# Kernel optimization log

Measured on AMD Instinct MI355X. Metric: run time of the kernel, lower is better.

## Reference

```python
import jax, jax.numpy as jnp
import numpy as np

STRIDE = 16
PRE_K = 600
POST_K = 100
NMS_T = 0.7


def _gen_anchors(base=16.0, ratios=(0.5, 1.0, 2.0), scales=(8.0, 16.0, 32.0)):
    a = []
    for s in scales:
        for r in ratios:
            w = base * s * (r ** 0.5)
            h = base * s / (r ** 0.5)
            a.append([-w / 2, -h / 2, w / 2, h / 2])
    return jnp.asarray(a, jnp.float32)  # [9,4]


def _conv(x, w, b, pad):
    y = jax.lax.conv_general_dilated(x, w, (1, 1), [(pad, pad), (pad, pad)],
                                     dimension_numbers=("NCHW", "OIHW", "NCHW"))
    return y + b[None, :, None, None]


def _decode(deltas, anchors):
    w = anchors[:, 2] - anchors[:, 0]
    h = anchors[:, 3] - anchors[:, 1]
    cx = anchors[:, 0] + 0.5 * w
    cy = anchors[:, 1] + 0.5 * h
    dx, dy, dw, dh = deltas[:, 0], deltas[:, 1], deltas[:, 2], deltas[:, 3]
    pcx = cx + dx * w
    pcy = cy + dy * h
    pw = w * jnp.exp(dw)
    ph = h * jnp.exp(dh)
    return jnp.stack([pcx - 0.5 * pw, pcy - 0.5 * ph,
                      pcx + 0.5 * pw, pcy + 0.5 * ph], axis=-1)


def _nms_keep(boxes, thresh):
    # boxes already sorted by score descending; returns bool keep mask [N]
    x1, y1, x2, y2 = boxes[:, 0], boxes[:, 1], boxes[:, 2], boxes[:, 3]
    area = (x2 - x1) * (y2 - y1)
    xx1 = jnp.maximum(x1[:, None], x1[None, :])
    yy1 = jnp.maximum(y1[:, None], y1[None, :])
    xx2 = jnp.minimum(x2[:, None], x2[None, :])
    yy2 = jnp.minimum(y2[:, None], y2[None, :])
    inter = jnp.maximum(xx2 - xx1, 0.0) * jnp.maximum(yy2 - yy1, 0.0)
    iou = inter / (area[:, None] + area[None, :] - inter)
    n = boxes.shape[0]
    idx = jnp.arange(n)

    def body(i, keep):
        suppress = keep[i] & (iou[i] > thresh) & (idx > i)
        return keep & ~suppress

    return jax.lax.fori_loop(0, n, body, jnp.ones((n,), bool))


def setup_inputs() -> dict:
    key = jax.random.key(0)
    ks = jax.random.split(key, 7)
    C_in, C_mid, A = 256, 256, 9
    feats = jax.random.normal(ks[0], (4, C_in, 128, 128), jnp.float32)
    conv_w = jax.random.normal(ks[1], (C_mid, C_in, 3, 3), jnp.float32) * 0.02
    conv_b = jnp.zeros((C_mid,), jnp.float32)
    cls_w = jax.random.normal(ks[2], (A, C_mid, 1, 1), jnp.float32) * 0.05
    cls_b = jnp.zeros((A,), jnp.float32)
    bbox_w = jax.random.normal(ks[3], (A * 4, C_mid, 1, 1), jnp.float32) * 0.02
    bbox_b = jnp.zeros((A * 4,), jnp.float32)
    return {"features": feats, "conv_w": conv_w, "conv_b": conv_b,
            "cls_w": cls_w, "cls_b": cls_b, "bbox_w": bbox_w, "bbox_b": bbox_b,
            "image_h": 2048, "image_w": 2048}


def reference(features, conv_w, conv_b, cls_w, cls_b, bbox_w, bbox_b, image_h, image_w):
    B, _, H, W = features.shape
    A = cls_w.shape[0]
    t = jax.nn.relu(_conv(features, conv_w, conv_b, 1))
    logits = _conv(t, cls_w, cls_b, 0)        # [B,A,H,W]
    bbox_deltas = _conv(t, bbox_w, bbox_b, 0)  # [B,4A,H,W]

    anchors = _gen_anchors()
    sx = jnp.arange(W, dtype=jnp.float32) * STRIDE
    sy = jnp.arange(H, dtype=jnp.float32) * STRIDE
    gy, gx = jnp.meshgrid(sy, sx, indexing="ij")
    shifts = jnp.stack([gx, gy, gx, gy], axis=2).reshape(-1, 4)  # [HW,4]
    anchors_all = (anchors[None, :, :] + shifts[:, None, :]).reshape(-1, 4)  # [HW*A,4]

    scores = jnp.transpose(logits, (0, 2, 3, 1)).reshape(B, -1)          # [B,HWA]
    deltas = jnp.transpose(bbox_deltas, (0, 2, 3, 1)).reshape(B, -1, 4)  # [B,HWA,4]

    img_w = jnp.float32(image_w)
    img_h = jnp.float32(image_h)

    def per_image(s, d):
        p = _decode(d, anchors_all)
        p = jnp.stack([jnp.clip(p[:, 0], 0.0, img_w),
                       jnp.clip(p[:, 1], 0.0, img_h),
                       jnp.clip(p[:, 2], 0.0, img_w),
                       jnp.clip(p[:, 3], 0.0, img_h)], axis=-1)
        _, topi = jax.lax.top_k(s, PRE_K)
        p = p[topi]                                # [PRE_K,4] sorted by score
        keep = _nms_keep(p, NMS_T)
        order = jnp.argsort(jnp.where(keep, 0, 1), stable=True)  # kept first, score order
        sel = order[:POST_K]
        valid = keep[sel]
        return p[sel] * valid[:, None].astype(p.dtype)  # zero-pad suppressed slots

    return jax.vmap(per_image)(scores, deltas)  # [B,POST_K,4]
```

## Files before the change

kernel.cpp:

```cpp
#include <hip/hip_runtime.h>
#include <cstdint>
#include <cstddef>

#define BB 4
#define CIN 256
#define HH 128
#define WW 128
#define NANCH (HH*WW*9)
#define PRE_K 600
#define POST_K 100
#define NMS_T 0.7f
#define CAND_CAP 8192
#define CCNT_STRIDE 16

typedef _Float16 f16x8 __attribute__((ext_vector_type(8)));
typedef float    f32x4 __attribute__((ext_vector_type(4)));

#define WS_SCORES 0
#define WS_DELTAS (BB*NANCH)
#define WS_WHI    (WS_DELTAS + BB*NANCH*4)
#define WS_WLO    (WS_WHI + 9*256*128)
#define WS_HIST   (WS_WLO + 9*256*128)
#define WS_CCNT   (WS_HIST + 8192)
#define WS_CAND   (WS_CCNT + 64)
#define WS_BOX6   (WS_CAND + BB*CAND_CAP*2)
#define WS_MROW   (WS_BOX6 + BB*PRE_K*4)
#define WS_PHI    (WS_MROW + BB*PRE_K*10*2)
#define WS_PLANE_F 8388608
#define WS_PLO    (WS_PHI + WS_PLANE_F)
#define WS_ZERO   (WS_PLO + WS_PLANE_F)
#define WS_TOTAL_FULL (WS_ZERO + 16)
#define WS_TOTAL_MIN  WS_PHI

__device__ inline unsigned score_key(float f) {
    unsigned u = __float_as_uint(f);
    return (u & 0x80000000u) ? ~u : (u | 0x80000000u);
}

__device__ inline void decode_box(unsigned idx, const float* __restrict__ deltas,
                                  int b, float fw, float fh, float* o4)
{
    const int a   = (int)(idx % 9u);
    const int n4  = (int)(idx / 9u);
    const int hh_ = n4 >> 7;
    const int ww_ = n4 & 127;
    const int si_ = a / 3, ri = a % 3;
    const double sq = (ri == 0) ? 0.70710678118654752440 : ((ri == 1) ? 1.0 : 1.41421356237309504880);
    const double sc = (si_ == 0) ? 8.0 : ((si_ == 1) ? 16.0 : 32.0);
    const float half_w = (float)(16.0 * sc * sq * 0.5);
    const float half_h = (float)(16.0 * sc / sq * 0.5);
    const float shx = 16.f * (float)ww_;
    const float shy = 16.f * (float)hh_;
    const float x1a = shx - half_w, x2a = shx + half_w;
    const float y1a = shy - half_h, y2a = shy + half_h;
    const float aw = x2a - x1a, ah = y2a - y1a;
    const float acx = x1a + 0.5f*aw, acy = y1a + 0.5f*ah;
    const float* d = deltas + ((size_t)b*NANCH + idx) * 4;
    const float dx = d[0], dy = d[1], dw = d[2], dh = d[3];
    const float pcx = acx + dx*aw;
    const float pcy = acy + dy*ah;
    const float pw  = aw * expf(dw);
    const float ph  = ah * expf(dh);
    o4[0] = fminf(fmaxf(pcx - 0.5f*pw, 0.f), fw);
    o4[1] = fminf(fmaxf(pcy - 0.5f*ph, 0.f), fh);
    o4[2] = fminf(fmaxf(pcx + 0.5f*pw, 0.f), fw);
    o4[3] = fminf(fmaxf(pcy + 0.5f*ph, 0.f), fh);
}

__global__ __launch_bounds__(256)
void prep_all(const float* __restrict__ feat, const float* __restrict__ convw,
              _Float16* __restrict__ pHi, _Float16* __restrict__ pLo,
              _Float16* __restrict__ whi, _Float16* __restrict__ wlo,
              float* __restrict__ zeroPg, unsigned* __restrict__ ghist,
              int prepBlocks)
{
    const int blk = blockIdx.x;
    if (blk < prepBlocks) {
        const int id = blk * 256 + threadIdx.x;
        if (blk == 0 && threadIdx.x < 16) zeroPg[threadIdx.x] = 0.f;
        const int gx = id & 127;
        const int gy = (id >> 7) & 127;
        const int ck = (id >> 14) & 7;
        const int b  = id >> 17;
        const int g  = (((gx + 1) >> 1) & 1) | (((gy + 1) & 1) << 1);
        const float* fb = feat + ((size_t)(b*256 + ck*32) << 14) + (gy << 7) + gx;
        f16x8 gh[4], gl[4];
        #pragma unroll
        for (int icg = 0; icg < 4; ++icg)
            #pragma unroll
            for (int k = 0; k < 8; ++k) {
                const float v = fb[(size_t)(icg*8 + k) << 14] * 16.f;
                const _Float16 h = (_Float16)v;
                gh[icg][k] = h;
                gl[icg][k] = (_Float16)(v - (float)h);
            }
        char* Hc = (char*)pHi + (size_t)id * 64;
        char* Lc = (char*)pLo + (size_t)id * 64;
        #pragma unroll
        for (int icg = 0; icg < 4; ++icg) {
            const int p = icg ^ g;
            *(f16x8*)(Hc + p*16) = gh[icg];
            *(f16x8*)(Lc + p*16) = gl[icg];
        }
    } else if (blk < prepBlocks + 256) {
        const int g = (blk - prepBlocks) * 256 + threadIdx.x;
        if (g >= 65536) return;
        const int oc = g >> 8, ic = g & 255;
        const int chunk = ic >> 5, icl = ic & 31;
        #pragma unroll
        for (int t = 0; t < 9; ++t) {
            const float v = convw[(size_t)g*9 + t] * 64.f;
            const _Float16 h = (_Float16)v;
            const _Float16 lo = (_Float16)(v - (float)h);
            const size_t o = (size_t)((t*8 + chunk)*256 + oc)*32 + icl;
            whi[o] = h;
            wlo[o] = lo;
        }
    } else {
        const int id = (blk - prepBlocks - 256) * 256 + threadIdx.x;
        if (id < 8256) ghist[id] = 0u;
    }
}

__global__ __launch_bounds__(512, 2)
void conv_mfma(const float* __restrict__ feat, const float* __restrict__ convb,
               const _Float16* __restrict__ whi, const _Float16* __restrict__ wlo,
               const float* __restrict__ clsw, const float* __restrict__ bboxw,
               const float* __restrict__ clsb, const float* __restrict__ bboxb,
               const _Float16* __restrict__ pHi, const _Float16* __restrict__ pLo,
               const float* __restrict__ zeroPg, unsigned* __restrict__ ghist,
               float* __restrict__ scores, float* __restrict__ deltas)
{
    __shared__ __align__(16) unsigned char smem[87040];
    float* sBias = (float*)(smem + 86016);

    const int bid = blockIdx.x;
    const int b  = bid >> 6;
    const int ty = (bid >> 3) & 7;
    const int tx = bid & 7;
    const int h0 = ty*16, c0 = tx*16;
    const int tid = threadIdx.x;
    const int w   = tid >> 6;
    const int wm  = w >> 1;
    const int wph = w & 1;
    const int l  = tid & 63;
    const int q  = l >> 4;
    const int c  = l & 15;

    const float* featb = feat + (size_t)b*CIN*HH*WW;
    const int wOff = (wm*64 + c)*32 + q*8;

    if (tid < 256) sBias[tid] = convb[tid] * 1024.f;

    int sdesc[3];
    #pragma unroll
    for (int it = 0; it < 3; ++it) {
        const int e = it*512 + tid;
        if (e < 1344) {
            const int Yl = e / 72, rem = e - Yl*72;
            const int Xl = rem >> 2, p = rem & 3;
            const int gy = h0 - 1 + Yl, gx = c0 - 1 + Xl;
            sdesc[it] = (((unsigned)gy < 128u) && ((unsigned)gx < 128u))
                        ? ((((gy << 7) + gx) << 6) + (p << 4)) : -1;
        } else sdesc[it] = -2;
    }

    auto stage = [&](int ck, int buf) {
        unsigned char* hb = smem + buf*21504;
        unsigned char* lb = smem + 43008 + buf*21504;
        if (pHi) {
            const size_t pb = ((size_t)(b*8 + ck)) << 20;
            #pragma unroll
            for (int pl = 0; pl < 2; ++pl) {
                const char* Ps = (const char*)(pl ? pLo : pHi) + pb;
                unsigned char* Pd = pl ? lb : hb;
                #pragma unroll
                for (int it = 0; it < 3; ++it) {
                    if (sdesc[it] != -2) {
                        const char* src = (sdesc[it] >= 0) ? Ps + sdesc[it]
                                                           : (const char*)zeroPg;
                        __builtin_amdgcn_global_load_lds(
                            (const __attribute__((address_space(1))) void*)src,
                            (__attribute__((address_space(3))) void*)(Pd + it*8192 + tid*16),
                            16, 0, 0);
                    }
                }
            }
        } else {
            const int ic0s = ck*32;
            for (int e = tid; e < 1296; e += 512) {
                const int icg = e / 324, s = e - icg*324;
                const int Y = s / 18, X = s - Y*18;
                const int gy = h0 - 1 + Y, gx = c0 - 1 + X;
                const int g = ((X >> 1) & 1) | ((Y & 1) << 1);
                const bool inb = ((unsigned)gy < 128u) && ((unsigned)gx < 128u);
                f16x8 hv, lv;
                #pragma unroll
                for (int k = 0; k < 8; ++k) {
                    float v = 0.f;
                    if (inb) v = featb[((size_t)(ic0s + icg*8 + k)*HH + gy)*WW + gx];
                    v *= 16.f;
                    const _Float16 h = (_Float16)v;
                    hv[k] = h;
                    lv[k] = (_Float16)(v - (float)h);
                }
                const int base = s*64 + ((icg ^ g) << 4);
                *(f16x8*)(hb + base) = hv;
                *(f16x8*)(lb + base) = lv;
            }
        }
    };

    stage(0, 0);
    __syncthreads();

    f32x4 acc[4][8];
    #pragma unroll
    for (int mf = 0; mf < 4; ++mf) {
        const f32x4 bv = *(const f32x4*)(sBias + (wm*64 + mf*16 + 4*q));
        #pragma unroll
        for (int nf = 0; nf < 8; ++nf) acc[mf][nf] = bv;
    }

    for (int chunk = 0; chunk < 8; ++chunk) {
        const int cur = chunk & 1;
        if (chunk + 1 < 8) stage(chunk + 1, cur ^ 1);
        const unsigned char* hb = smem + cur*21504;
        const unsigned char* lb = smem + 43008 + cur*21504;

        #pragma unroll 3
        for (int t = 0; t < 9; ++t) {
            const int ky = t / 3, kx = t - ky*3;
            const _Float16* pWh = whi + (size_t)(t*8 + chunk)*8192 + wOff;
            const _Float16* pWl = wlo + (size_t)(t*8 + chunk)*8192 + wOff;
            f16x8 ah[4], al[4];
            #pragma unroll
            for (int mf = 0; mf < 4; ++mf) {
                ah[mf] = *(const f16x8*)(const void*)(pWh + mf*512);
                al[mf] = *(const f16x8*)(const void*)(pWl + mf*512);
            }
            #pragma unroll
            for (int nfh = 0; nfh < 2; ++nfh) {
                f16x8 bh[4], bl[4];
                #pragma unroll
                for (int j = 0; j < 4; ++j) {
                    const int nf = nfh*4 + j;
                    const int Y = wph*8 + (nf >> 1)*2 + (c >> 3) + ky;
                    const int X = (nf & 1)*8 + (c & 7) + kx;
                    const int g = ((X >> 1) & 1) | ((Y & 1) << 1);
                    const int addr = (Y*18 + X)*64 + ((q ^ g) << 4);
                    bh[j] = *(const f16x8*)(hb + addr);
                    bl[j] = *(const f16x8*)(lb + addr);
                }
                #pragma unroll
                for (int mf = 0; mf < 4; ++mf)
                    #pragma unroll
                    for (int j = 0; j < 4; ++j) {
                        acc[mf][nfh*4+j] = __builtin_amdgcn_mfma_f32_16x16x32_f16(ah[mf], bh[j], acc[mf][nfh*4+j], 0, 0, 0);
                        acc[mf][nfh*4+j] = __builtin_amdgcn_mfma_f32_16x16x32_f16(ah[mf], bl[j], acc[mf][nfh*4+j], 0, 0, 0);
                        acc[mf][nfh*4+j] = __builtin_amdgcn_mfma_f32_16x16x32_f16(al[mf], bh[j], acc[mf][nfh*4+j], 0, 0, 0);
                    }
            }
        }
        __syncthreads();
    }

    #pragma unroll
    for (int mf = 0; mf < 4; ++mf)
        #pragma unroll
        for (int nf = 0; nf < 8; ++nf)
            #pragma unroll
            for (int r = 0; r < 4; ++r)
                acc[mf][nf][r] = fmaxf(acc[mf][nf][r], 0.f) * 0.0009765625f;

    float*    sW15  = (float*)smem;
    float*    sPart = (float*)(smem + 15360);
    unsigned* sHist = (unsigned*)(smem + 76800);

    for (int e = tid; e < 2048; e += 512) sHist[e] = 0u;

    for (int g = 0; g < 3; ++g) {
        __syncthreads();
        for (int e = tid; e < 3840; e += 512) {
            const int chl = e >> 8, o = e & 255;
            const int ch = g*15 + chl;
            sW15[e] = (ch < 9) ? clsw[ch*256 + o] : bboxw[(ch - 9)*256 + o];
        }
        __syncthreads();
        for (int chl = 0; chl < 15; ++chl) {
            f32x4 wv[4];
            #pragma unroll
            for (int mf = 0; mf < 4; ++mf)
                wv[mf] = *(const f32x4*)(sW15 + chl*256 + wm*64 + mf*16 + 4*q);
            float p[8];
            #pragma unroll
            for (int nf = 0; nf < 8; ++nf) {
                float s = 0.f;
                #pragma unroll
                for (int mf = 0; mf < 4; ++mf)
                    #pragma unroll
                    for (int r = 0; r < 4; ++r)
                        s += wv[mf][r] * acc[mf][nf][r];
                s += __shfl_xor(s, 16, 64);
                s += __shfl_xor(s, 32, 64);
                p[nf] = s;
            }
            const float v0 = (q == 0) ? p[0] : (q == 1) ? p[1] : (q == 2) ? p[2] : p[3];
            const float v1 = (q == 0) ? p[4] : (q == 1) ? p[5] : (q == 2) ? p[6] : p[7];
            sPart[(w*15 + chl)*128 + q*16 + c]      = v0;
            sPart[(w*15 + chl)*128 + 64 + q*16 + c] = v1;
        }
        __syncthreads();
        for (int e = tid; e < 3840; e += 512) {
            const int chl = e >> 8, pxg = e & 255;
            const int ph = pxg >> 7, pxl = pxg & 127;
            float s = 0.f;
            #pragma unroll
            for (int wmq = 0; wmq < 4; ++wmq)
                s += sPart[((wmq*2 + ph)*15 + chl)*128 + pxl];
            const int ch = g*15 + chl;
            s += (ch < 9) ? clsb[ch] : bboxb[ch - 9];
            const int nf = pxl >> 4, cc2 = pxl & 15;
            const int Y = ph*8 + (nf >> 1)*2 + (cc2 >> 3);
            const int X = (nf & 1)*8 + (cc2 & 7);
            const int gy = h0 + Y, gx = c0 + X;
            const int n4 = gy*WW + gx;
            if (ch < 9) {
                scores[(size_t)b*NANCH + n4*9 + ch] = s;
                atomicAdd(&sHist[score_key(s) >> 21], 1u);
            } else {
                const int cc = ch - 9;
                deltas[((size_t)b*NANCH + n4*9 + (cc >> 2))*4 + (cc & 3)] = s;
            }
        }
    }
    for (int e = tid; e < 2048; e += 512) {
        const unsigned cv = sHist[e];
        if (cv) atomicAdd(&ghist[b*2048 + e], cv);
    }
}

__device__ inline void find_thresh(const unsigned* hist, int NB, unsigned target, unsigned* shv)
{
    const int tid = threadIdx.x;
    if (tid < 64) {
        const int gsz = NB >> 5;
        unsigned gsum = 0;
        if (tid < 32)
            for (int k = 0; k < gsz; ++k)
                gsum += hist[tid*gsz + ((k + tid) & (gsz-1))];
        unsigned suf = gsum;
        #pragma unroll
        for (int d = 1; d < 32; d <<= 1) {
            const unsigned t = __shfl_down(suf, d, 64);
            if (tid + d < 32) suf += t;
        }
        const unsigned long long m = __ballot(tid < 32 && suf >= target);
        const int G = 63 - __clzll(m);
        unsigned caboveG = 0;
        { const unsigned t = __shfl(suf, G+1, 64); if (G < 31) caboveG = t; }
        unsigned h = 0;
        if (tid < gsz) h = hist[G*gsz + tid];
        unsigned wsuf = h;
        #pragma unroll
        for (int d = 1; d < 64; d <<= 1) {
            const unsigned t = __shfl_down(wsuf, d, 64);
            if (tid + d < gsz) wsuf += t;
        }
        const unsigned long long m2 = __ballot(tid < gsz && (caboveG + wsuf) >= target);
        const int L = 63 - __clzll(m2);
        if (tid == L) { shv[0] = (unsigned)(G*gsz + L); shv[1] = caboveG + wsuf - h; }
    }
}

__global__ __launch_bounds__(256)
void filter_kernel(const float* __restrict__ scores, const unsigned* __restrict__ ghist,
                   unsigned* __restrict__ ccnt, unsigned long long* __restrict__ cand)
{
    __shared__ unsigned h[2048];
    __shared__ unsigned shv[8];
    __shared__ unsigned long long lbuf[2304];
    __shared__ unsigned lcnt, gbase;
    const int blk = blockIdx.x;
    const int b = blk >> 6, s = blk & 63;
    const int tid = threadIdx.x;
    const unsigned* hb = ghist + b*2048;
    if (tid == 0) lcnt = 0u;
    for (int e = tid; e < 2048; e += 256) h[e] = hb[e];
    __syncthreads();
    find_thresh(h, 2048, PRE_K, shv);
    __syncthreads();
    const unsigned T1 = shv[0];
    const unsigned C  = shv[1] + h[T1];
    const float* si = scores + (size_t)b*NANCH + s*2304;
    if (C <= (unsigned)CAND_CAP) {
        #pragma unroll
        for (int k = 0; k < 9; ++k) {
            const int i = tid + k*256;
            const unsigned u = score_key(si[i]);
            if ((u >> 21) >= T1) {
                const unsigned p = atomicAdd(&lcnt, 1u);
                lbuf[p] = ((unsigned long long)(~u) << 32) | (unsigned)(s*2304 + i);
            }
        }
        __syncthreads();
        if (tid == 0) gbase = atomicAdd(&ccnt[b*CCNT_STRIDE], lcnt);
        __syncthreads();
        const unsigned nL = lcnt, base = gbase;
        for (unsigned e = tid; e < nL; e += 256)
            cand[(size_t)b*CAND_CAP + base + e] = lbuf[e];
    } else if (s == 0 && tid == 0) {
        ccnt[b*CCNT_STRIDE] = 0x7FFFFFFFu;
    }
}

__global__ __launch_bounds__(256)
void rank_kernel(const unsigned* __restrict__ ccnt, const unsigned long long* __restrict__ cand,
                 const float* __restrict__ deltas,
                 const int* __restrict__ imh, const int* __restrict__ imw,
                 float* __restrict__ boxes6)
{
    __shared__ unsigned long long cnd[CAND_CAP];
    const int blk = blockIdx.x;
    const int b = blk >> 5, s = blk & 31;
    const int tid = threadIdx.x;
    const unsigned n = ccnt[b*CCNT_STRIDE];
    if (n > (unsigned)CAND_CAP) return;
    const int e0 = s*256;
    if ((unsigned)e0 >= n) return;
    for (int e = tid; e < (int)n; e += 256)
        cnd[e] = cand[(size_t)b*CAND_CAP + e];
    __syncthreads();
    const int e = e0 + tid;
    if (e >= (int)n) return;
    const unsigned long long cv = cnd[e];
    unsigned rank = 0;
    for (int e2 = 0; e2 < (int)n; ++e2)
        rank += (cnd[e2] < cv) ? 1u : 0u;
    if (rank < PRE_K) {
        float o4[4];
        decode_box((unsigned)cv, deltas, b, (float)imw[0], (float)imh[0], o4);
        float* o = boxes6 + ((size_t)b*PRE_K + rank)*4;
        o[0] = o4[0]; o[1] = o4[1]; o[2] = o4[2]; o[3] = o4[3];
    }
}

__global__ __launch_bounds__(256)
void nmsmask_kernel(const unsigned* __restrict__ ccnt, const float* __restrict__ boxes6,
                    unsigned long long* __restrict__ gmrow)
{
    __shared__ float bx[PRE_K][4];
    const int blk = blockIdx.x;
    const int b = blk / 10, rg = blk - b*10;
    const int tid = threadIdx.x;
    const unsigned n = ccnt[b*CCNT_STRIDE];
    if (n > (unsigned)CAND_CAP) return;
    for (int e = tid; e < PRE_K*4; e += 256)
        bx[e >> 2][e & 3] = boxes6[(size_t)b*PRE_K*4 + e];
    __syncthreads();
    for (int item = tid; item < 600; item += 256) {
        const int i  = rg*60 + item/10;
        const int wj = item - (item/10)*10;
        unsigned long long m = 0ull;
        const int jbase = wj * 64;
        if (jbase + 63 > i) {
            const float xi1 = bx[i][0], yi1 = bx[i][1], xi2 = bx[i][2], yi2 = bx[i][3];
            const float ai = (xi2 - xi1) * (yi2 - yi1);
            for (int bit = 0; bit < 64; ++bit) {
                const int j = jbase + bit;
                if (j < PRE_K && j > i) {
                    const float xx1 = fmaxf(xi1, bx[j][0]);
                    const float yy1 = fmaxf(yi1, bx[j][1]);
                    const float xx2 = fminf(xi2, bx[j][2]);
                    const float yy2 = fminf(yi2, bx[j][3]);
                    const float inter = fmaxf(xx2 - xx1, 0.f) * fmaxf(yy2 - yy1, 0.f);
                    const float aj = (bx[j][2] - bx[j][0]) * (bx[j][3] - bx[j][1]);
                    const float iou = inter / (ai + aj - inter);
                    if (iou > NMS_T) m |= (1ull << bit);
                }
            }
        }
        gmrow[((size_t)b*PRE_K + i)*10 + wj] = m;
    }
}

__device__ inline unsigned long long shfl_u64(unsigned long long v, int src) {
    const int lo = __shfl((int)(v & 0xffffffffull), src, 64);
    const int hi = __shfl((int)(v >> 32), src, 64);
    return ((unsigned long long)(unsigned)hi << 32) | (unsigned)lo;
}

__global__ __launch_bounds__(1024)
void post_kernel(const float* __restrict__ scores, const float* __restrict__ deltas,
                 const unsigned* __restrict__ ccnt,
                 const float* __restrict__ boxes6, const unsigned long long* __restrict__ gmrow,
                 const int* __restrict__ imh, const int* __restrict__ imw,
                 float* __restrict__ out)
{
    __shared__ unsigned hist[2048];
    __shared__ unsigned long long arr[1024];
    __shared__ unsigned tiebuf[1024];
    __shared__ unsigned shv[8];
    __shared__ float bx[PRE_K][4];
    __shared__ unsigned long long mrow[PRE_K][10];
    __shared__ unsigned long long keepw[10];
    __shared__ unsigned wpfx[11];
    __shared__ int sel[POST_K];
    const int b = blockIdx.x, tid = threadIdx.x;
    const float* si = scores + (size_t)b*NANCH;

    const unsigned n = ccnt[b*CCNT_STRIDE];
    const bool fast = (n <= (unsigned)CAND_CAP);

    if (fast) {
        for (int e = tid; e < PRE_K*4; e += 1024)
            bx[e >> 2][e & 3] = boxes6[(size_t)b*PRE_K*4 + e];
        for (int e = tid; e < PRE_K*10; e += 1024)
            mrow[e/10][e - (e/10)*10] = gmrow[(size_t)b*PRE_K*10 + e];
        __syncthreads();
    } else {
        for (int i = tid; i < 2048; i += 1024) hist[i] = 0;
        __syncthreads();
        for (int i = tid; i < NANCH; i += 1024)
            atomicAdd(&hist[score_key(si[i]) >> 21], 1u);
        __syncthreads();
        find_thresh(hist, 2048, PRE_K, shv);
        __syncthreads();
        const unsigned T1 = shv[0], gtA = shv[1];
        __syncthreads();

        for (int i = tid; i < 2048; i += 1024) hist[i] = 0;
        __syncthreads();
        for (int i = tid; i < NANCH; i += 1024) {
            const unsigned u = score_key(si[i]);
            if ((u >> 21) == T1) atomicAdd(&hist[(u >> 10) & 0x7FFu], 1u);
        }
        __syncthreads();
        find_thresh(hist, 2048, PRE_K - gtA, shv);
        __syncthreads();
        const unsigned T2 = shv[0], gtB = shv[1];
        const unsigned top22 = (T1 << 11) | T2;
        __syncthreads();

        for (int i = tid; i < 1024; i += 1024) hist[i] = 0;
        __syncthreads();
        for (int i = tid; i < NANCH; i += 1024) {
            const unsigned u = score_key(si[i]);
            if ((u >> 10) == top22) atomicAdd(&hist[u & 0x3FFu], 1u);
        }
        __syncthreads();
        find_thresh(hist, 1024, PRE_K - gtA - gtB, shv);
        if (tid == 0) { shv[4] = 0; shv[5] = 0; }
        __syncthreads();
        const unsigned u_thr = (top22 << 10) | shv[0];
        const unsigned n_greater = gtA + gtB + shv[1];
        __syncthreads();

        for (int i = tid; i < NANCH; i += 1024) {
            const unsigned u = score_key(si[i]);
            if (u > u_thr) {
                const unsigned p = atomicAdd(&shv[4], 1u);
                arr[p] = ((unsigned long long)(~u) << 32) | (unsigned)i;
            } else if (u == u_thr) {
                const unsigned p = atomicAdd(&shv[5], 1u);
                if (p < 1024u) tiebuf[p] = (unsigned)i;
            }
        }
        __syncthreads();
        const unsigned cnt_tie = (shv[5] > 1024u) ? 1024u : shv[5];
        if ((unsigned)tid >= cnt_tie) tiebuf[tid] = 0xFFFFFFFFu;

        for (unsigned k = 2; k <= 1024; k <<= 1)
            for (unsigned j = k >> 1; j > 0; j >>= 1) {
                __syncthreads();
                const unsigned i = (unsigned)tid, ixj = i ^ j;
                if (ixj > i) {
                    const unsigned a = tiebuf[i], cc = tiebuf[ixj];
                    if ((a > cc) == ((i & k) == 0)) { tiebuf[i] = cc; tiebuf[ixj] = a; }
                }
            }
        __syncthreads();
        const unsigned ties_needed = PRE_K - n_greater;
        if ((unsigned)tid < ties_needed)
            arr[n_greater + tid] = ((unsigned long long)(~u_thr) << 32) | tiebuf[tid];
        if (tid >= PRE_K) arr[tid] = ~0ull;

        for (unsigned k = 2; k <= 1024; k <<= 1)
            for (unsigned j = k >> 1; j > 0; j >>= 1) {
                __syncthreads();
                const unsigned i = (unsigned)tid, ixj = i ^ j;
                if (ixj > i) {
                    const unsigned long long a = arr[i], cc = arr[ixj];
                    if ((a > cc) == ((i & k) == 0)) { arr[i] = cc; arr[ixj] = a; }
                }
            }
        __syncthreads();

        if (tid < PRE_K) {
            float o4[4];
            decode_box((unsigned)arr[tid], deltas, b, (float)imw[0], (float)imh[0], o4);
            bx[tid][0] = o4[0]; bx[tid][1] = o4[1]; bx[tid][2] = o4[2]; bx[tid][3] = o4[3];
        }
        __syncthreads();

        for (int item = tid; item < PRE_K*10; item += 1024) {
            const int i  = item / 10;
            const int wj = item - i*10;
            unsigned long long m = 0ull;
            const int jbase = wj * 64;
            if (jbase + 63 > i) {
                const float xi1 = bx[i][0], yi1 = bx[i][1], xi2 = bx[i][2], yi2 = bx[i][3];
                const float ai = (xi2 - xi1) * (yi2 - yi1);
                for (int bit = 0; bit < 64; ++bit) {
                    const int j = jbase + bit;
                    if (j < PRE_K && j > i) {
                        const float xx1 = fmaxf(xi1, bx[j][0]);
                        const float yy1 = fmaxf(yi1, bx[j][1]);
                        const float xx2 = fminf(xi2, bx[j][2]);
                        const float yy2 = fminf(yi2, bx[j][3]);
                        const float inter = fmaxf(xx2 - xx1, 0.f) * fmaxf(yy2 - yy1, 0.f);
                        const float aj = (bx[j][2] - bx[j][0]) * (bx[j][3] - bx[j][1]);
                        const float iou = inter / (ai + aj - inter);
                        if (iou > NMS_T) m |= (1ull << bit);
                    }
                }
            }
            mrow[i][wj] = m;
        }
        __syncthreads();
    }

    if (tid < 64) {
        const int lane = tid;
        unsigned long long kwv;
        if (lane < 9)       kwv = ~0ull;
        else if (lane == 9) kwv = (1ull << (PRE_K - 576)) - 1;
        else                kwv = 0ull;
        for (int w = 0; w < 10; ++w) {
            const int base = w*64;
            const int nb = (w == 9) ? (PRE_K - 576) : 64;
            if (lane == w) {
                for (int bit = 0; bit < nb; ++bit) {
                    const unsigned long long mm = mrow[base + bit][w];
                    if ((kwv >> bit) & 1ull) kwv &= ~mm;
                }
            }
            const unsigned long long fw = shfl_u64(kwv, w);
            if (lane > w && lane < 10) {
                for (int bit = 0; bit < nb; ++bit) {
                    const unsigned long long mm = mrow[base + bit][lane];
                    if ((fw >> bit) & 1ull) kwv &= ~mm;
                }
            }
        }
        if (lane < 10) keepw[lane] = kwv;
    }
    __syncthreads();
    if (tid == 0) {
        unsigned ccount = 0;
        #pragma unroll
        for (int w = 0; w < 10; ++w) { wpfx[w] = ccount; ccount += (unsigned)__popcll(keepw[w]); }
        wpfx[10] = ccount;
    }
    if (tid < POST_K) sel[tid] = -1;
    __syncthreads();
    if (tid < PRE_K) {
        const int w = tid >> 6, bit = tid & 63;
        const unsigned long long kw = keepw[w];
        if ((kw >> bit) & 1ull) {
            const unsigned rank = wpfx[w] + (unsigned)__popcll(kw & ((1ull << bit) - 1ull));
            if (rank < POST_K) sel[rank] = tid;
        }
    }
    __syncthreads();
    if (tid < POST_K) {
        const int s_ = sel[tid];
        float o0 = 0.f, o1 = 0.f, o2 = 0.f, o3 = 0.f;
        if (s_ >= 0) { o0 = bx[s_][0]; o1 = bx[s_][1]; o2 = bx[s_][2]; o3 = bx[s_][3]; }
        float* o = out + (size_t)b*POST_K*4 + tid*4;
        o[0] = o0; o[1] = o1; o[2] = o2; o[3] = o3;
    }
}

extern "C" void kernel_launch(void* const* d_in, const int* in_sizes, int n_in,
                              void* d_out, int out_size, void* d_ws, size_t ws_size,
                              hipStream_t stream) {
    const float* feat  = (const float*)d_in[0];
    const float* convw = (const float*)d_in[1];
    const float* convb = (const float*)d_in[2];
    const float* clsw  = (const float*)d_in[3];
    const float* clsb  = (const float*)d_in[4];
    const float* bboxw = (const float*)d_in[5];
    const float* bboxb = (const float*)d_in[6];
    const int*   imh   = (const int*)d_in[7];
    const int*   imw   = (const int*)d_in[8];

    if (ws_size < (size_t)WS_TOTAL_MIN * sizeof(float)) return;
    const bool use_prep = ws_size >= (size_t)WS_TOTAL_FULL * sizeof(float);

    float*    scores = (float*)d_ws + WS_SCORES;
    float*    deltas = (float*)d_ws + WS_DELTAS;
    _Float16* whi    = (_Float16*)((float*)d_ws + WS_WHI);
    _Float16* wlo    = (_Float16*)((float*)d_ws + WS_WLO);
    unsigned* ghist  = (unsigned*)((float*)d_ws + WS_HIST);
    unsigned* ccnt   = (unsigned*)((float*)d_ws + WS_CCNT);
    unsigned long long* cand = (unsigned long long*)((float*)d_ws + WS_CAND);
    float*    boxes6 = (float*)d_ws + WS_BOX6;
    unsigned long long* gmrow = (unsigned long long*)((float*)d_ws + WS_MROW);
    _Float16* pHi    = use_prep ? (_Float16*)((float*)d_ws + WS_PHI) : nullptr;
    _Float16* pLo    = use_prep ? (_Float16*)((float*)d_ws + WS_PLO) : nullptr;
    float*    zeroPg = use_prep ? ((float*)d_ws + WS_ZERO) : nullptr;
    float*    outp   = (float*)d_out;

    const int prepBlocks = use_prep ? 2048 : 0;
    prep_all<<<dim3(prepBlocks + 256 + 33), dim3(256), 0, stream>>>(
        feat, convw, pHi, pLo, whi, wlo, zeroPg, ghist, prepBlocks);
    conv_mfma<<<dim3(256), dim3(512), 0, stream>>>(feat, convb, whi, wlo, clsw, bboxw,
                                                   clsb, bboxb, pHi, pLo, zeroPg, ghist,
                                                   scores, deltas);
    filter_kernel<<<dim3(256), dim3(256), 0, stream>>>(scores, ghist, ccnt, cand);
    rank_kernel<<<dim3(128), dim3(256), 0, stream>>>(ccnt, cand, deltas, imh, imw, boxes6);
    nmsmask_kernel<<<dim3(40), dim3(256), 0, stream>>>(ccnt, boxes6, gmrow);
    post_kernel<<<dim3(BB), dim3(1024), 0, stream>>>(scores, deltas, ccnt, boxes6, gmrow,
                                                     imh, imw, outp);
}
```

Baseline: 359.2 us.

## Fuse filter, rank, NMS-mask and post kernels into one cooperative kernel

```diff
diff --git a/kernel.cpp b/kernel.cpp
--- a/kernel.cpp
+++ b/kernel.cpp
@@ -1,6 +1,9 @@
 #include <hip/hip_runtime.h>
+#include <hip/hip_cooperative_groups.h>
 #include <cstdint>
 #include <cstddef>
+
+namespace cg = cooperative_groups;
 
 #define BB 4
 #define CIN 256
@@ -373,312 +376,315 @@
     }
 }
 
-__global__ __launch_bounds__(256)
-void filter_kernel(const float* __restrict__ scores, const unsigned* __restrict__ ghist,
-                   unsigned* __restrict__ ccnt, unsigned long long* __restrict__ cand)
-{
-    __shared__ unsigned h[2048];
-    __shared__ unsigned shv[8];
-    __shared__ unsigned long long lbuf[2304];
-    __shared__ unsigned lcnt, gbase;
-    const int blk = blockIdx.x;
-    const int b = blk >> 6, s = blk & 63;
-    const int tid = threadIdx.x;
-    const unsigned* hb = ghist + b*2048;
-    if (tid == 0) lcnt = 0u;
-    for (int e = tid; e < 2048; e += 256) h[e] = hb[e];
-    __syncthreads();
-    find_thresh(h, 2048, PRE_K, shv);
-    __syncthreads();
-    const unsigned T1 = shv[0];
-    const unsigned C  = shv[1] + h[T1];
-    const float* si = scores + (size_t)b*NANCH + s*2304;
-    if (C <= (unsigned)CAND_CAP) {
-        #pragma unroll
-        for (int k = 0; k < 9; ++k) {
-            const int i = tid + k*256;
-            const unsigned u = score_key(si[i]);
-            if ((u >> 21) >= T1) {
-                const unsigned p = atomicAdd(&lcnt, 1u);
-                lbuf[p] = ((unsigned long long)(~u) << 32) | (unsigned)(s*2304 + i);
-            }
-        }
-        __syncthreads();
-        if (tid == 0) gbase = atomicAdd(&ccnt[b*CCNT_STRIDE], lcnt);
-        __syncthreads();
-        const unsigned nL = lcnt, base = gbase;
-        for (unsigned e = tid; e < nL; e += 256)
-            cand[(size_t)b*CAND_CAP + base + e] = lbuf[e];
-    } else if (s == 0 && tid == 0) {
-        ccnt[b*CCNT_STRIDE] = 0x7FFFFFFFu;
-    }
-}
-
-__global__ __launch_bounds__(256)
-void rank_kernel(const unsigned* __restrict__ ccnt, const unsigned long long* __restrict__ cand,
-                 const float* __restrict__ deltas,
-                 const int* __restrict__ imh, const int* __restrict__ imw,
-                 float* __restrict__ boxes6)
-{
-    __shared__ unsigned long long cnd[CAND_CAP];
-    const int blk = blockIdx.x;
-    const int b = blk >> 5, s = blk & 31;
-    const int tid = threadIdx.x;
-    const unsigned n = ccnt[b*CCNT_STRIDE];
-    if (n > (unsigned)CAND_CAP) return;
-    const int e0 = s*256;
-    if ((unsigned)e0 >= n) return;
-    for (int e = tid; e < (int)n; e += 256)
-        cnd[e] = cand[(size_t)b*CAND_CAP + e];
-    __syncthreads();
-    const int e = e0 + tid;
-    if (e >= (int)n) return;
-    const unsigned long long cv = cnd[e];
-    unsigned rank = 0;
-    for (int e2 = 0; e2 < (int)n; ++e2)
-        rank += (cnd[e2] < cv) ? 1u : 0u;
-    if (rank < PRE_K) {
-        float o4[4];
-        decode_box((unsigned)cv, deltas, b, (float)imw[0], (float)imh[0], o4);
-        float* o = boxes6 + ((size_t)b*PRE_K + rank)*4;
-        o[0] = o4[0]; o[1] = o4[1]; o[2] = o4[2]; o[3] = o4[3];
-    }
-}
-
-__global__ __launch_bounds__(256)
-void nmsmask_kernel(const unsigned* __restrict__ ccnt, const float* __restrict__ boxes6,
-                    unsigned long long* __restrict__ gmrow)
-{
-    __shared__ float bx[PRE_K][4];
-    const int blk = blockIdx.x;
-    const int b = blk / 10, rg = blk - b*10;
-    const int tid = threadIdx.x;
-    const unsigned n = ccnt[b*CCNT_STRIDE];
-    if (n > (unsigned)CAND_CAP) return;
-    for (int e = tid; e < PRE_K*4; e += 256)
-        bx[e >> 2][e & 3] = boxes6[(size_t)b*PRE_K*4 + e];
-    __syncthreads();
-    for (int item = tid; item < 600; item += 256) {
-        const int i  = rg*60 + item/10;
-        const int wj = item - (item/10)*10;
-        unsigned long long m = 0ull;
-        const int jbase = wj * 64;
-        if (jbase + 63 > i) {
-            const float xi1 = bx[i][0], yi1 = bx[i][1], xi2 = bx[i][2], yi2 = bx[i][3];
-            const float ai = (xi2 - xi1) * (yi2 - yi1);
-            for (int bit = 0; bit < 64; ++bit) {
-                const int j = jbase + bit;
-                if (j < PRE_K && j > i) {
-                    const float xx1 = fmaxf(xi1, bx[j][0]);
-                    const float yy1 = fmaxf(yi1, bx[j][1]);
-                    const float xx2 = fminf(xi2, bx[j][2]);
-                    const float yy2 = fminf(yi2, bx[j][3]);
-                    const float inter = fmaxf(xx2 - xx1, 0.f) * fmaxf(yy2 - yy1, 0.f);
-                    const float aj = (bx[j][2] - bx[j][0]) * (bx[j][3] - bx[j][1]);
-                    const float iou = inter / (ai + aj - inter);
-                    if (iou > NMS_T) m |= (1ull << bit);
-                }
-            }
-        }
-        gmrow[((size_t)b*PRE_K + i)*10 + wj] = m;
-    }
-}
-
 __device__ inline unsigned long long shfl_u64(unsigned long long v, int src) {
     const int lo = __shfl((int)(v & 0xffffffffull), src, 64);
     const int hi = __shfl((int)(v >> 32), src, 64);
     return ((unsigned long long)(unsigned)hi << 32) | (unsigned)lo;
 }
 
-__global__ __launch_bounds__(1024)
-void post_kernel(const float* __restrict__ scores, const float* __restrict__ deltas,
-                 const unsigned* __restrict__ ccnt,
-                 const float* __restrict__ boxes6, const unsigned long long* __restrict__ gmrow,
+__global__ __launch_bounds__(256)
+void tail_kernel(const float* __restrict__ scores, const unsigned* __restrict__ ghist,
+                 unsigned* __restrict__ ccnt, unsigned long long* __restrict__ cand,
+                 const float* __restrict__ deltas, float* __restrict__ boxes6,
+                 unsigned long long* __restrict__ gmrow,
                  const int* __restrict__ imh, const int* __restrict__ imw,
                  float* __restrict__ out)
 {
-    __shared__ unsigned hist[2048];
-    __shared__ unsigned long long arr[1024];
-    __shared__ unsigned tiebuf[1024];
-    __shared__ unsigned shv[8];
-    __shared__ float bx[PRE_K][4];
-    __shared__ unsigned long long mrow[PRE_K][10];
-    __shared__ unsigned long long keepw[10];
-    __shared__ unsigned wpfx[11];
-    __shared__ int sel[POST_K];
-    const int b = blockIdx.x, tid = threadIdx.x;
-    const float* si = scores + (size_t)b*NANCH;
-
-    const unsigned n = ccnt[b*CCNT_STRIDE];
-    const bool fast = (n <= (unsigned)CAND_CAP);
-
-    if (fast) {
-        for (int e = tid; e < PRE_K*4; e += 1024)
-            bx[e >> 2][e & 3] = boxes6[(size_t)b*PRE_K*4 + e];
-        for (int e = tid; e < PRE_K*10; e += 1024)
-            mrow[e/10][e - (e/10)*10] = gmrow[(size_t)b*PRE_K*10 + e];
-        __syncthreads();
-    } else {
-        for (int i = tid; i < 2048; i += 1024) hist[i] = 0;
-        __syncthreads();
-        for (int i = tid; i < NANCH; i += 1024)
-            atomicAdd(&hist[score_key(si[i]) >> 21], 1u);
-        __syncthreads();
-        find_thresh(hist, 2048, PRE_K, shv);
-        __syncthreads();
-        const unsigned T1 = shv[0], gtA = shv[1];
-        __syncthreads();
-
-        for (int i = tid; i < 2048; i += 1024) hist[i] = 0;
-        __syncthreads();
-        for (int i = tid; i < NANCH; i += 1024) {
-            const unsigned u = score_key(si[i]);
-            if ((u >> 21) == T1) atomicAdd(&hist[(u >> 10) & 0x7FFu], 1u);
-        }
-        __syncthreads();
-        find_thresh(hist, 2048, PRE_K - gtA, shv);
-        __syncthreads();
-        const unsigned T2 = shv[0], gtB = shv[1];
-        const unsigned top22 = (T1 << 11) | T2;
-        __syncthreads();
-
-        for (int i = tid; i < 1024; i += 1024) hist[i] = 0;
-        __syncthreads();
-        for (int i = tid; i < NANCH; i += 1024) {
-            const unsigned u = score_key(si[i]);
-            if ((u >> 10) == top22) atomicAdd(&hist[u & 0x3FFu], 1u);
-        }
-        __syncthreads();
-        find_thresh(hist, 1024, PRE_K - gtA - gtB, shv);
-        if (tid == 0) { shv[4] = 0; shv[5] = 0; }
-        __syncthreads();
-        const unsigned u_thr = (top22 << 10) | shv[0];
-        const unsigned n_greater = gtA + gtB + shv[1];
-        __syncthreads();
-
-        for (int i = tid; i < NANCH; i += 1024) {
-            const unsigned u = score_key(si[i]);
-            if (u > u_thr) {
-                const unsigned p = atomicAdd(&shv[4], 1u);
-                arr[p] = ((unsigned long long)(~u) << 32) | (unsigned)i;
-            } else if (u == u_thr) {
-                const unsigned p = atomicAdd(&shv[5], 1u);
-                if (p < 1024u) tiebuf[p] = (unsigned)i;
-            }
-        }
-        __syncthreads();
-        const unsigned cnt_tie = (shv[5] > 1024u) ? 1024u : shv[5];
-        if ((unsigned)tid >= cnt_tie) tiebuf[tid] = 0xFFFFFFFFu;
-
-        for (unsigned k = 2; k <= 1024; k <<= 1)
-            for (unsigned j = k >> 1; j > 0; j >>= 1) {
+    __shared__ __align__(16) unsigned char tsm[81920];
+    cg::grid_group grid = cg::this_grid();
+    const int blk = blockIdx.x, tid = threadIdx.x;
+
+    {
+        unsigned* h = (unsigned*)tsm;
+        unsigned long long* lbuf = (unsigned long long*)(tsm + 8192);
+        unsigned* ctl = (unsigned*)(tsm + 26624);
+        const int b = blk >> 6, s = blk & 63;
+        if (tid == 0) ctl[8] = 0u;
+        const unsigned* hb = ghist + b*2048;
+        for (int e = tid; e < 2048; e += 256) h[e] = hb[e];
+        __syncthreads();
+        find_thresh(h, 2048, PRE_K, ctl);
+        __syncthreads();
+        const unsigned T1 = ctl[0];
+        const unsigned C  = ctl[1] + h[T1];
+        const float* si = scores + (size_t)b*NANCH + s*2304;
+        if (C <= (unsigned)CAND_CAP) {
+            #pragma unroll
+            for (int k = 0; k < 9; ++k) {
+                const int i = tid + k*256;
+                const unsigned u = score_key(si[i]);
+                if ((u >> 21) >= T1) {
+                    const unsigned p = atomicAdd(&ctl[8], 1u);
+                    lbuf[p] = ((unsigned long long)(~u) << 32) | (unsigned)(s*2304 + i);
+                }
+            }
+            __syncthreads();
+            if (tid == 0) ctl[9] = atomicAdd(&ccnt[b*CCNT_STRIDE], ctl[8]);
+            __syncthreads();
+            const unsigned nL = ctl[8], base = ctl[9];
+            for (unsigned e = tid; e < nL; e += 256)
+                cand[(size_t)b*CAND_CAP + base + e] = lbuf[e];
+        } else if (s == 0 && tid == 0) {
+            ccnt[b*CCNT_STRIDE] = 0x7FFFFFFFu;
+        }
+    }
+    grid.sync();
+
+    {
+        unsigned long long* cnd = (unsigned long long*)tsm;
+        if (blk < 128) {
+            const int b = blk >> 5, s = blk & 31;
+            const unsigned n = ccnt[b*CCNT_STRIDE];
+            if (n <= (unsigned)CAND_CAP && (unsigned)(s*256) < n) {
+                for (int e = tid; e < (int)n; e += 256)
+                    cnd[e] = cand[(size_t)b*CAND_CAP + e];
                 __syncthreads();
-                const unsigned i = (unsigned)tid, ixj = i ^ j;
-                if (ixj > i) {
-                    const unsigned a = tiebuf[i], cc = tiebuf[ixj];
-                    if ((a > cc) == ((i & k) == 0)) { tiebuf[i] = cc; tiebuf[ixj] = a; }
-                }
-            }
-        __syncthreads();
-        const unsigned ties_needed = PRE_K - n_greater;
-        if ((unsigned)tid < ties_needed)
-            arr[n_greater + tid] = ((unsigned long long)(~u_thr) << 32) | tiebuf[tid];
-        if (tid >= PRE_K) arr[tid] = ~0ull;
-
-        for (unsigned k = 2; k <= 1024; k <<= 1)
-            for (unsigned j = k >> 1; j > 0; j >>= 1) {
+                const int e = s*256 + tid;
+                if (e < (int)n) {
+                    const unsigned long long cv = cnd[e];
+                    unsigned rank = 0;
+                    for (int e2 = 0; e2 < (int)n; ++e2)
+                        rank += (cnd[e2] < cv) ? 1u : 0u;
+                    if (rank < PRE_K) {
+                        float o4[4];
+                        decode_box((unsigned)cv, deltas, b, (float)imw[0], (float)imh[0], o4);
+                        float* o = boxes6 + ((size_t)b*PRE_K + rank)*4;
+                        o[0] = o4[0]; o[1] = o4[1]; o[2] = o4[2]; o[3] = o4[3];
+                    }
+                }
+            }
+        }
+    }
+    grid.sync();
+
+    {
+        float* bx = (float*)tsm;
+        if (blk < 40) {
+            const int b = blk / 10, rg = blk - b*10;
+            const unsigned n = ccnt[b*CCNT_STRIDE];
+            if (n <= (unsigned)CAND_CAP) {
+                for (int e = tid; e < PRE_K*4; e += 256)
+                    bx[e] = boxes6[(size_t)b*PRE_K*4 + e];
                 __syncthreads();
-                const unsigned i = (unsigned)tid, ixj = i ^ j;
-                if (ixj > i) {
-                    const unsigned long long a = arr[i], cc = arr[ixj];
-                    if ((a > cc) == ((i & k) == 0)) { arr[i] = cc; arr[ixj] = a; }
-                }
-            }
-        __syncthreads();
-
-        if (tid < PRE_K) {
-            float o4[4];
-            decode_box((unsigned)arr[tid], deltas, b, (float)imw[0], (float)imh[0], o4);
-            bx[tid][0] = o4[0]; bx[tid][1] = o4[1]; bx[tid][2] = o4[2]; bx[tid][3] = o4[3];
-        }
-        __syncthreads();
-
-        for (int item = tid; item < PRE_K*10; item += 1024) {
-            const int i  = item / 10;
-            const int wj = item - i*10;
-            unsigned long long m = 0ull;
-            const int jbase = wj * 64;
-            if (jbase + 63 > i) {
-                const float xi1 = bx[i][0], yi1 = bx[i][1], xi2 = bx[i][2], yi2 = bx[i][3];
-                const float ai = (xi2 - xi1) * (yi2 - yi1);
-                for (int bit = 0; bit < 64; ++bit) {
-                    const int j = jbase + bit;
-                    if (j < PRE_K && j > i) {
-                        const float xx1 = fmaxf(xi1, bx[j][0]);
-                        const float yy1 = fmaxf(yi1, bx[j][1]);
-                        const float xx2 = fminf(xi2, bx[j][2]);
-                        const float yy2 = fminf(yi2, bx[j][3]);
-                        const float inter = fmaxf(xx2 - xx1, 0.f) * fmaxf(yy2 - yy1, 0.f);
-                        const float aj = (bx[j][2] - bx[j][0]) * (bx[j][3] - bx[j][1]);
-                        const float iou = inter / (ai + aj - inter);
-                        if (iou > NMS_T) m |= (1ull << bit);
-                    }
-                }
-            }
-            mrow[i][wj] = m;
-        }
-        __syncthreads();
-    }
-
-    if (tid < 64) {
-        const int lane = tid;
-        unsigned long long kwv;
-        if (lane < 9)       kwv = ~0ull;
-        else if (lane == 9) kwv = (1ull << (PRE_K - 576)) - 1;
-        else                kwv = 0ull;
-        for (int w = 0; w < 10; ++w) {
-            const int base = w*64;
-            const int nb = (w == 9) ? (PRE_K - 576) : 64;
-            if (lane == w) {
-                for (int bit = 0; bit < nb; ++bit) {
-                    const unsigned long long mm = mrow[base + bit][w];
-                    if ((kwv >> bit) & 1ull) kwv &= ~mm;
-                }
-            }
-            const unsigned long long fw = shfl_u64(kwv, w);
-            if (lane > w && lane < 10) {
-                for (int bit = 0; bit < nb; ++bit) {
-                    const unsigned long long mm = mrow[base + bit][lane];
-                    if ((fw >> bit) & 1ull) kwv &= ~mm;
-                }
-            }
-        }
-        if (lane < 10) keepw[lane] = kwv;
-    }
-    __syncthreads();
-    if (tid == 0) {
-        unsigned ccount = 0;
-        #pragma unroll
-        for (int w = 0; w < 10; ++w) { wpfx[w] = ccount; ccount += (unsigned)__popcll(keepw[w]); }
-        wpfx[10] = ccount;
-    }
-    if (tid < POST_K) sel[tid] = -1;
-    __syncthreads();
-    if (tid < PRE_K) {
-        const int w = tid >> 6, bit = tid & 63;
-        const unsigned long long kw = keepw[w];
-        if ((kw >> bit) & 1ull) {
-            const unsigned rank = wpfx[w] + (unsigned)__popcll(kw & ((1ull << bit) - 1ull));
-            if (rank < POST_K) sel[rank] = tid;
-        }
-    }
-    __syncthreads();
-    if (tid < POST_K) {
-        const int s_ = sel[tid];
-        float o0 = 0.f, o1 = 0.f, o2 = 0.f, o3 = 0.f;
-        if (s_ >= 0) { o0 = bx[s_][0]; o1 = bx[s_][1]; o2 = bx[s_][2]; o3 = bx[s_][3]; }
-        float* o = out + (size_t)b*POST_K*4 + tid*4;
-        o[0] = o0; o[1] = o1; o[2] = o2; o[3] = o3;
+                for (int item = tid; item < 600; item += 256) {
+                    const int i  = rg*60 + item/10;
+                    const int wj = item - (item/10)*10;
+                    unsigned long long m = 0ull;
+                    const int jbase = wj * 64;
+                    if (jbase + 63 > i) {
+                        const float xi1 = bx[i*4+0], yi1 = bx[i*4+1], xi2 = bx[i*4+2], yi2 = bx[i*4+3];
+                        const float ai = (xi2 - xi1) * (yi2 - yi1);
+                        for (int bit = 0; bit < 64; ++bit) {
+                            const int j = jbase + bit;
+                            if (j < PRE_K && j > i) {
+                                const float xx1 = fmaxf(xi1, bx[j*4+0]);
+                                const float yy1 = fmaxf(yi1, bx[j*4+1]);
+                                const float xx2 = fminf(xi2, bx[j*4+2]);
+                                const float yy2 = fminf(yi2, bx[j*4+3]);
+                                const float inter = fmaxf(xx2 - xx1, 0.f) * fmaxf(yy2 - yy1, 0.f);
+                                const float aj = (bx[j*4+2] - bx[j*4+0]) * (bx[j*4+3] - bx[j*4+1]);
+                                const float iou = inter / (ai + aj - inter);
+                                if (iou > NMS_T) m |= (1ull << bit);
+                            }
+                        }
+                    }
+                    gmrow[((size_t)b*PRE_K + i)*10 + wj] = m;
+                }
+            }
+        }
+    }
+    grid.sync();
+
+    if (blk < 4) {
+        const int b = blk;
+        float* bx = (float*)tsm;
+        unsigned long long* mrow = (unsigned long long*)(tsm + 9600);
+        unsigned long long* keepw = (unsigned long long*)(tsm + 57600);
+        unsigned* wpfx = (unsigned*)(tsm + 57728);
+        int* sel = (int*)(tsm + 57792);
+        const unsigned n = ccnt[b*CCNT_STRIDE];
+        const bool fast = (n <= (unsigned)CAND_CAP);
+
+        if (fast) {
+            for (int e = tid; e < PRE_K*4; e += 256)
+                bx[e] = boxes6[(size_t)b*PRE_K*4 + e];
+            for (int e = tid; e < PRE_K*10; e += 256)
+                mrow[e] = gmrow[(size_t)b*PRE_K*10 + e];
+            __syncthreads();
+        } else {
+            unsigned* hist = (unsigned*)(tsm + 58240);
+            unsigned long long* arr = (unsigned long long*)(tsm + 66432);
+            unsigned* tiebuf = (unsigned*)(tsm + 74624);
+            unsigned* shv = (unsigned*)(tsm + 78720);
+            const float* si = scores + (size_t)b*NANCH;
+
+            for (int i = tid; i < 2048; i += 256) hist[i] = 0;
+            __syncthreads();
+            for (int i = tid; i < NANCH; i += 256)
+                atomicAdd(&hist[score_key(si[i]) >> 21], 1u);
+            __syncthreads();
+            find_thresh(hist, 2048, PRE_K, shv);
+            __syncthreads();
+            const unsigned T1 = shv[0], gtA = shv[1];
+            __syncthreads();
+
+            for (int i = tid; i < 2048; i += 256) hist[i] = 0;
+            __syncthreads();
+            for (int i = tid; i < NANCH; i += 256) {
+                const unsigned u = score_key(si[i]);
+                if ((u >> 21) == T1) atomicAdd(&hist[(u >> 10) & 0x7FFu], 1u);
+            }
+            __syncthreads();
+            find_thresh(hist, 2048, PRE_K - gtA, shv);
+            __syncthreads();
+            const unsigned T2 = shv[0], gtB = shv[1];
+            const unsigned top22 = (T1 << 11) | T2;
+            __syncthreads();
+
+            for (int i = tid; i < 1024; i += 256) hist[i] = 0;
+            __syncthreads();
+            for (int i = tid; i < NANCH; i += 256) {
+                const unsigned u = score_key(si[i]);
+                if ((u >> 10) == top22) atomicAdd(&hist[u & 0x3FFu], 1u);
+            }
+            __syncthreads();
+            find_thresh(hist, 1024, PRE_K - gtA - gtB, shv);
+            if (tid == 0) { shv[4] = 0; shv[5] = 0; }
+            __syncthreads();
+            const unsigned u_thr = (top22 << 10) | shv[0];
+            const unsigned n_greater = gtA + gtB + shv[1];
+            __syncthreads();
+
+            for (int i = tid; i < NANCH; i += 256) {
+                const unsigned u = score_key(si[i]);
+                if (u > u_thr) {
+                    const unsigned p = atomicAdd(&shv[4], 1u);
+                    arr[p] = ((unsigned long long)(~u) << 32) | (unsigned)i;
+                } else if (u == u_thr) {
+                    const unsigned p = atomicAdd(&shv[5], 1u);
+                    if (p < 1024u) tiebuf[p] = (unsigned)i;
+                }
+            }
+            __syncthreads();
+            const unsigned cnt_tie = (shv[5] > 1024u) ? 1024u : shv[5];
+            for (int i = tid; i < 1024; i += 256)
+                if ((unsigned)i >= cnt_tie) tiebuf[i] = 0xFFFFFFFFu;
+
+            for (unsigned k = 2; k <= 1024; k <<= 1)
+                for (unsigned j = k >> 1; j > 0; j >>= 1) {
+                    __syncthreads();
+                    for (int i0 = tid; i0 < 1024; i0 += 256) {
+                        const unsigned i = (unsigned)i0, ixj = i ^ j;
+                        if (ixj > i) {
+                            const unsigned a = tiebuf[i], cc = tiebuf[ixj];
+                            if ((a > cc) == ((i & k) == 0)) { tiebuf[i] = cc; tiebuf[ixj] = a; }
+                        }
+                    }
+                }
+            __syncthreads();
+            const unsigned ties_needed = PRE_K - n_greater;
+            for (int i = tid; i < (int)ties_needed; i += 256)
+                arr[n_greater + i] = ((unsigned long long)(~u_thr) << 32) | tiebuf[i];
+            for (int i = tid; i < 1024; i += 256)
+                if (i >= PRE_K) arr[i] = ~0ull;
+
+            for (unsigned k = 2; k <= 1024; k <<= 1)
+                for (unsigned j = k >> 1; j > 0; j >>= 1) {
+                    __syncthreads();
+                    for (int i0 = tid; i0 < 1024; i0 += 256) {
+                        const unsigned i = (unsigned)i0, ixj = i ^ j;
+                        if (ixj > i) {
+                            const unsigned long long a = arr[i], cc = arr[ixj];
+                            if ((a > cc) == ((i & k) == 0)) { arr[i] = cc; arr[ixj] = a; }
+                        }
+                    }
+                }
+            __syncthreads();
+
+            for (int i = tid; i < PRE_K; i += 256) {
+                float o4[4];
+                decode_box((unsigned)arr[i], deltas, b, (float)imw[0], (float)imh[0], o4);
+                bx[i*4+0] = o4[0]; bx[i*4+1] = o4[1]; bx[i*4+2] = o4[2]; bx[i*4+3] = o4[3];
+            }
+            __syncthreads();
+
+            for (int item = tid; item < PRE_K*10; item += 256) {
+                const int i  = item / 10;
+                const int wj = item - i*10;
+                unsigned long long m = 0ull;
+                const int jbase = wj * 64;
+                if (jbase + 63 > i) {
+                    const float xi1 = bx[i*4+0], yi1 = bx[i*4+1], xi2 = bx[i*4+2], yi2 = bx[i*4+3];
+                    const float ai = (xi2 - xi1) * (yi2 - yi1);
+                    for (int bit = 0; bit < 64; ++bit) {
+                        const int j = jbase + bit;
+                        if (j < PRE_K && j > i) {
+                            const float xx1 = fmaxf(xi1, bx[j*4+0]);
+                            const float yy1 = fmaxf(yi1, bx[j*4+1]);
+                            const float xx2 = fminf(xi2, bx[j*4+2]);
+                            const float yy2 = fminf(yi2, bx[j*4+3]);
+                            const float inter = fmaxf(xx2 - xx1, 0.f) * fmaxf(yy2 - yy1, 0.f);
+                            const float aj = (bx[j*4+2] - bx[j*4+0]) * (bx[j*4+3] - bx[j*4+1]);
+                            const float iou = inter / (ai + aj - inter);
+                            if (iou > NMS_T) m |= (1ull << bit);
+                        }
+                    }
+                }
+                mrow[i*10 + wj] = m;
+            }
+            __syncthreads();
+        }
+
+        if (tid < 64) {
+            const int lane = tid;
+            unsigned long long kwv;
+            if (lane < 9)       kwv = ~0ull;
+            else if (lane == 9) kwv = (1ull << (PRE_K - 576)) - 1;
+            else                kwv = 0ull;
+            for (int w = 0; w < 10; ++w) {
+                const int base = w*64;
+                const int nb = (w == 9) ? (PRE_K - 576) : 64;
+                if (lane == w) {
+                    for (int bit = 0; bit < nb; ++bit) {
+                        const unsigned long long mm = mrow[(base + bit)*10 + w];
+                        if ((kwv >> bit) & 1ull) kwv &= ~mm;
+                    }
+                }
+                const unsigned long long fw = shfl_u64(kwv, w);
+                if (lane > w && lane < 10) {
+                    for (int bit = 0; bit < nb; ++bit) {
+                        const unsigned long long mm = mrow[(base + bit)*10 + lane];
+                        if ((fw >> bit) & 1ull) kwv &= ~mm;
+                    }
+                }
+            }
+            if (lane < 10) keepw[lane] = kwv;
+        }
+        __syncthreads();
+        if (tid == 0) {
+            unsigned ccount = 0;
+            #pragma unroll
+            for (int w = 0; w < 10; ++w) { wpfx[w] = ccount; ccount += (unsigned)__popcll(keepw[w]); }
+            wpfx[10] = ccount;
+        }
+        if (tid < POST_K) sel[tid] = -1;
+        __syncthreads();
+        for (int i = tid; i < PRE_K; i += 256) {
+            const int w = i >> 6, bit = i & 63;
+            const unsigned long long kw = keepw[w];
+            if ((kw >> bit) & 1ull) {
+                const unsigned rank = wpfx[w] + (unsigned)__popcll(kw & ((1ull << bit) - 1ull));
+                if (rank < POST_K) sel[rank] = i;
+            }
+        }
+        __syncthreads();
+        if (tid < POST_K) {
+            const int s_ = sel[tid];
+            float o0 = 0.f, o1 = 0.f, o2 = 0.f, o3 = 0.f;
+            if (s_ >= 0) { o0 = bx[s_*4+0]; o1 = bx[s_*4+1]; o2 = bx[s_*4+2]; o3 = bx[s_*4+3]; }
+            float* o = out + (size_t)b*POST_K*4 + tid*4;
+            o[0] = o0; o[1] = o1; o[2] = o2; o[3] = o3;
+        }
     }
 }
 
@@ -718,9 +724,9 @@
     conv_mfma<<<dim3(256), dim3(512), 0, stream>>>(feat, convb, whi, wlo, clsw, bboxw,
                                                    clsb, bboxb, pHi, pLo, zeroPg, ghist,
                                                    scores, deltas);
-    filter_kernel<<<dim3(256), dim3(256), 0, stream>>>(scores, ghist, ccnt, cand);
-    rank_kernel<<<dim3(128), dim3(256), 0, stream>>>(ccnt, cand, deltas, imh, imw, boxes6);
-    nmsmask_kernel<<<dim3(40), dim3(256), 0, stream>>>(ccnt, boxes6, gmrow);
-    post_kernel<<<dim3(BB), dim3(1024), 0, stream>>>(scores, deltas, ccnt, boxes6, gmrow,
-                                                     imh, imw, outp);
+    void* targs[10] = { (void*)&scores, (void*)&ghist, (void*)&ccnt, (void*)&cand,
+                        (void*)&deltas, (void*)&boxes6, (void*)&gmrow,
+                        (void*)&imh, (void*)&imw, (void*)&outp };
+    hipLaunchCooperativeKernel((const void*)tail_kernel, dim3(256), dim3(256),
+                               targs, 0, stream);
 }
```

Result: slower. 448.8 us (+24.9%).
